# Kernel optimization log

Measured on AMD Instinct MI355X. Metric: run time of the kernel, lower is better.

Reference implementation:

```python
import jax, jax.numpy as jnp
import numpy as np

TEMPERATURE = 1.0
B, D = 8192, 256


def setup_inputs() -> dict:
    key = jax.random.key(0)
    k1, k2 = jax.random.split(key)
    return {
        "encoder_embedding1": jax.random.normal(k1, (B, D), dtype=jnp.float32),
        "encoder_embedding2": jax.random.normal(k2, (B, D), dtype=jnp.float32),
    }


def _l2_normalize(x, eps=1e-8):
    # matches torch CosineSimilarity eps handling closely enough for fp32
    n = jnp.sqrt(jnp.sum(x * x, axis=-1, keepdims=True))
    return x / jnp.maximum(n, eps)


def reference(encoder_embedding1, encoder_embedding2):
    # sim[i, j] = cos(contrast_i, anchor_j); torch builds this via a (B,B,D)
    # expand + elementwise CosineSimilarity — here it's a normalized matmul.
    a = _l2_normalize(encoder_embedding1)  # anchors  [B, D]
    c = _l2_normalize(encoder_embedding2)  # contrast [B, D]
    sim = jnp.einsum("id,jd->ij", c, a)    # [B, B]
    log_probs = jax.nn.log_softmax(sim / TEMPERATURE, axis=0)
    loss = -jnp.sum(jnp.diagonal(log_probs)) * TEMPERATURE
    return loss
```

## Files before the change

kernel.cpp:

```cpp
#include <hip/hip_runtime.h>
#include <hip/hip_bf16.h>
#include <hip/hip_fp8.h>


#define BROWS 8192
#define DIM   256

typedef int   i32x4 __attribute__((ext_vector_type(4)));
typedef int   i32x8 __attribute__((ext_vector_type(8)));
typedef float f32x4 __attribute__((ext_vector_type(4)));

__device__ __forceinline__ void gload_lds16(const void* g, void* l) {
  __builtin_amdgcn_global_load_lds(
      (const __attribute__((address_space(1))) unsigned int*)g,
      (__attribute__((address_space(3))) unsigned int*)l, 16, 0, 0);
}

__device__ __forceinline__ unsigned char to_e4m3(float v) {
  __hip_fp8_e4m3 t(v);
  return *reinterpret_cast<unsigned char*>(&t);
}

__global__ __launch_bounds__(256) void prep_kernel(
    const float* __restrict__ E1, const float* __restrict__ E2,
    unsigned char* __restrict__ An8, unsigned char* __restrict__ Cn8,
    float* __restrict__ diag, float* __restrict__ colsum) {
  if (blockIdx.x < 32) colsum[blockIdx.x * 256 + threadIdx.x] = 0.f;

  const int w    = threadIdx.x >> 6;
  const int lane = threadIdx.x & 63;
  const int row  = blockIdx.x * 4 + w;
  const size_t base = (size_t)row * DIM + lane * 4;

  const float4 a = *(const float4*)(E1 + base);
  const float4 c = *(const float4*)(E2 + base);

  float sa  = a.x*a.x + a.y*a.y + a.z*a.z + a.w*a.w;
  float sc  = c.x*c.x + c.y*c.y + c.z*c.z + c.w*c.w;
  float sac = a.x*c.x + a.y*c.y + a.z*c.z + a.w*c.w;
#pragma unroll
  for (int o = 32; o > 0; o >>= 1) {
    sa  += __shfl_down(sa,  o);
    sc  += __shfl_down(sc,  o);
    sac += __shfl_down(sac, o);
  }
  const float inva = 1.0f / fmaxf(sqrtf(__shfl(sa, 0)), 1e-8f);
  const float invc = 1.0f / fmaxf(sqrtf(__shfl(sc, 0)), 1e-8f);

  uchar4 pa, pc;
  pa.x = to_e4m3(a.x * inva); pa.y = to_e4m3(a.y * inva);
  pa.z = to_e4m3(a.z * inva); pa.w = to_e4m3(a.w * inva);
  pc.x = to_e4m3(c.x * invc); pc.y = to_e4m3(c.y * invc);
  pc.z = to_e4m3(c.z * invc); pc.w = to_e4m3(c.w * invc);
  *(uchar4*)(An8 + base) = pa;
  *(uchar4*)(Cn8 + base) = pc;
  if (lane == 0) diag[row] = sac * inva * invc;
}

__global__ __launch_bounds__(256, 2) void gemm_colsum_kernel(
    const unsigned char* __restrict__ Cn8,
    const unsigned char* __restrict__ An8,
    float* __restrict__ colsum) {
  __shared__ __align__(16) unsigned char ldsC[32768];
  __shared__ __align__(16) unsigned char ldsA[4][2][4096];

  const int tid  = threadIdx.x;
  const int lane = tid & 63;
  const int w    = tid >> 6;
  const int ih   = w & 1;
  const int js   = w >> 1;

  const int jgroup = blockIdx.x & 31;
  const int itile  = blockIdx.x >> 5;
  const int i0 = itile * 128;
  const int j0 = jgroup * 256;
  const int jw = j0 + js * 128;

  const int sr = tid >> 4;
  const int pl = (tid & 15) ^ (sr & 7);
  const unsigned char* gC = Cn8 + (size_t)(i0 + sr) * DIM + pl * 16;
#pragma unroll
  for (int r = 0; r < 8; ++r)
    gload_lds16(gC + (size_t)(r * 16) * DIM, &ldsC[0] + r * 4096 + w * 1024);

  const int srow4 = lane >> 4;
  const int slot  = lane & 15;
  const unsigned char* gA0 = An8 + (size_t)srow4 * DIM + (slot ^ srow4) * 16;
  const unsigned char* gA1 = An8 + (size_t)srow4 * DIM + (slot ^ srow4 ^ 4) * 16;
  unsigned char* wbuf = &ldsA[w][0][0];

  auto stageA = [&](int jj, int buf) {
    const size_t cb = (size_t)(jw + jj * 16) * DIM;
    unsigned char* d = wbuf + buf * 4096;
#pragma unroll
    for (int r = 0; r < 4; ++r) {
      const unsigned char* s = (r & 1) ? gA1 : gA0;
      gload_lds16(s + cb + (size_t)(r * 4) * DIM, d + r * 1024);
    }
  };

  stageA(0, 0);
  stageA(1, 1);

  asm volatile("s_waitcnt vmcnt(8)" ::: "memory");
  __builtin_amdgcn_sched_barrier(0);
  __builtin_amdgcn_s_barrier();

  const int q  = lane >> 4;
  const int rb = lane & 15;
  const int SC = 0x7F7F7F7F;

  i32x8 af[4][2];
#pragma unroll
  for (int m = 0; m < 4; ++m) {
    const int r = ih * 64 + m * 16 + rb;
#pragma unroll
    for (int W = 0; W < 2; ++W) {
      const int s0 = (W * 8 + q * 2)     ^ (r & 7);
      const int s1 = (W * 8 + q * 2 + 1) ^ (r & 7);
      union { i32x4 h[2]; i32x8 v; } u;
      u.h[0] = *(const i32x4*)(&ldsC[0] + r * 256 + s0 * 16);
      u.h[1] = *(const i32x4*)(&ldsC[0] + r * 256 + s1 * 16);
      af[m][W] = u.v;
    }
  }
  asm volatile("s_waitcnt lgkmcnt(0)" ::: "memory");
  __builtin_amdgcn_sched_barrier(0);

#pragma unroll
  for (int jj = 0; jj < 8; ++jj) {
    const int b = jj & 1;
    if (jj == 0)      asm volatile("s_waitcnt vmcnt(4)" ::: "memory");
    else if (jj == 1) asm volatile("s_waitcnt vmcnt(5)" ::: "memory");
    else if (jj == 7) asm volatile("s_waitcnt vmcnt(2)" ::: "memory");
    else              asm volatile("s_waitcnt vmcnt(6)" ::: "memory");
    __builtin_amdgcn_sched_barrier(0);

    i32x8 bf[2];
#pragma unroll
    for (int W = 0; W < 2; ++W) {
      const int s0 = (W * 8 + q * 2)     ^ (rb & 7);
      const int s1 = (W * 8 + q * 2 + 1) ^ (rb & 7);
      union { i32x4 h[2]; i32x8 v; } u;
      u.h[0] = *(const i32x4*)(wbuf + b * 4096 + rb * 256 + s0 * 16);
      u.h[1] = *(const i32x4*)(wbuf + b * 4096 + rb * 256 + s1 * 16);
      bf[W] = u.v;
    }
    asm volatile("s_waitcnt lgkmcnt(0)" ::: "memory");
    __builtin_amdgcn_sched_barrier(0);

    if (jj < 6) stageA(jj + 2, b);
    __builtin_amdgcn_sched_barrier(0);

    f32x4 acc[4] = {};
    __builtin_amdgcn_s_setprio(1);
#pragma unroll
    for (int m = 0; m < 4; ++m)
#pragma unroll
      for (int W = 0; W < 2; ++W)
        acc[m] = __builtin_amdgcn_mfma_scale_f32_16x16x128_f8f6f4(
            af[m][W], bf[W], acc[m], 0, 0, 0, SC, 0, SC);
    __builtin_amdgcn_s_setprio(0);

    float s = 0.f;
#pragma unroll
    for (int m = 0; m < 4; ++m) {
      const f32x4 v = acc[m];
      s += __expf(v[0]) + __expf(v[1]) + __expf(v[2]) + __expf(v[3]);
    }
    s += __shfl_xor(s, 16);
    s += __shfl_xor(s, 32);
    if (lane < 16) atomicAdd(&colsum[jw + jj * 16 + lane], s);
  }
}

__global__ __launch_bounds__(256) void finalize_kernel(
    const float* __restrict__ colsum, const float* __restrict__ diag,
    float* __restrict__ out) {
  const int t = threadIdx.x;
  float s = 0.f;
  for (int j = t; j < BROWS; j += 256) s += logf(colsum[j]) - diag[j];
#pragma unroll
  for (int o = 32; o > 0; o >>= 1) s += __shfl_down(s, o);
  __shared__ float red[4];
  if ((t & 63) == 0) red[t >> 6] = s;
  __syncthreads();
  if (t == 0) out[0] = red[0] + red[1] + red[2] + red[3];
}

extern "C" void kernel_launch(void* const* d_in, const int* in_sizes, int n_in,
                              void* d_out, int out_size, void* d_ws, size_t ws_size,
                              hipStream_t stream) {
  const float* E1 = (const float*)d_in[0];
  const float* E2 = (const float*)d_in[1];
  char* ws = (char*)d_ws;
  unsigned char* Cn8 = (unsigned char*)(ws);
  unsigned char* An8 = (unsigned char*)(ws + (size_t)2 * 1024 * 1024);
  float* colsum = (float*)(ws + (size_t)4 * 1024 * 1024);
  float* diag   = (float*)(ws + (size_t)4 * 1024 * 1024 + 32 * 1024);
  float* out = (float*)d_out;

  prep_kernel<<<BROWS / 4, 256, 0, stream>>>(E1, E2, An8, Cn8, diag, colsum);
  gemm_colsum_kernel<<<64 * 32, 256, 0, stream>>>(Cn8, An8, colsum);
  finalize_kernel<<<1, 256, 0, stream>>>(colsum, diag, out);
}
```

Before: 50.84 us.

## Load MFMA operands directly from global memory into registers, dropping LDS staging

The GEMM kernel no longer stages the C tile and the A sub-tiles through LDS with async global-to-LDS loads and hand-placed waitcnts. Each lane now reads its fp8 fragments straight from global memory into registers, with register double-buffering for the B operand. This removes LDS traffic, the block barrier and the swizzle arithmetic, and lets the compiler schedule the waits. In exchange it gives up cross-wave sharing of the C tile, so global/L2 reads per block go up, and the launch-bounds occupancy hint is dropped.

```diff
diff --git a/kernel.cpp b/kernel.cpp
--- a/kernel.cpp
+++ b/kernel.cpp
@@ -6,15 +6,8 @@
 #define BROWS 8192
 #define DIM   256
 
-typedef int   i32x4 __attribute__((ext_vector_type(4)));
 typedef int   i32x8 __attribute__((ext_vector_type(8)));
 typedef float f32x4 __attribute__((ext_vector_type(4)));
-
-__device__ __forceinline__ void gload_lds16(const void* g, void* l) {
-  __builtin_amdgcn_global_load_lds(
-      (const __attribute__((address_space(1))) unsigned int*)g,
-      (__attribute__((address_space(3))) unsigned int*)l, 16, 0, 0);
-}
 
 __device__ __forceinline__ unsigned char to_e4m3(float v) {
   __hip_fp8_e4m3 t(v);
@@ -57,13 +50,10 @@
   if (lane == 0) diag[row] = sac * inva * invc;
 }
 
-__global__ __launch_bounds__(256, 2) void gemm_colsum_kernel(
+__global__ __launch_bounds__(256) void gemm_colsum_kernel(
     const unsigned char* __restrict__ Cn8,
     const unsigned char* __restrict__ An8,
     float* __restrict__ colsum) {
-  __shared__ __align__(16) unsigned char ldsC[32768];
-  __shared__ __align__(16) unsigned char ldsA[4][2][4096];
-
   const int tid  = threadIdx.x;
   const int lane = tid & 63;
   const int w    = tid >> 6;
@@ -73,85 +63,30 @@
   const int jgroup = blockIdx.x & 31;
   const int itile  = blockIdx.x >> 5;
   const int i0 = itile * 128;
-  const int j0 = jgroup * 256;
-  const int jw = j0 + js * 128;
-
-  const int sr = tid >> 4;
-  const int pl = (tid & 15) ^ (sr & 7);
-  const unsigned char* gC = Cn8 + (size_t)(i0 + sr) * DIM + pl * 16;
-#pragma unroll
-  for (int r = 0; r < 8; ++r)
-    gload_lds16(gC + (size_t)(r * 16) * DIM, &ldsC[0] + r * 4096 + w * 1024);
-
-  const int srow4 = lane >> 4;
-  const int slot  = lane & 15;
-  const unsigned char* gA0 = An8 + (size_t)srow4 * DIM + (slot ^ srow4) * 16;
-  const unsigned char* gA1 = An8 + (size_t)srow4 * DIM + (slot ^ srow4 ^ 4) * 16;
-  unsigned char* wbuf = &ldsA[w][0][0];
-
-  auto stageA = [&](int jj, int buf) {
-    const size_t cb = (size_t)(jw + jj * 16) * DIM;
-    unsigned char* d = wbuf + buf * 4096;
-#pragma unroll
-    for (int r = 0; r < 4; ++r) {
-      const unsigned char* s = (r & 1) ? gA1 : gA0;
-      gload_lds16(s + cb + (size_t)(r * 4) * DIM, d + r * 1024);
-    }
-  };
-
-  stageA(0, 0);
-  stageA(1, 1);
-
-  asm volatile("s_waitcnt vmcnt(8)" ::: "memory");
-  __builtin_amdgcn_sched_barrier(0);
-  __builtin_amdgcn_s_barrier();
+  const int jw = jgroup * 256 + js * 128;
 
   const int q  = lane >> 4;
   const int rb = lane & 15;
   const int SC = 0x7F7F7F7F;
 
+  const unsigned char* cb =
+      Cn8 + (size_t)(i0 + ih * 64 + rb) * DIM + q * 32;
   i32x8 af[4][2];
 #pragma unroll
-  for (int m = 0; m < 4; ++m) {
-    const int r = ih * 64 + m * 16 + rb;
+  for (int m = 0; m < 4; ++m)
 #pragma unroll
-    for (int W = 0; W < 2; ++W) {
-      const int s0 = (W * 8 + q * 2)     ^ (r & 7);
-      const int s1 = (W * 8 + q * 2 + 1) ^ (r & 7);
-      union { i32x4 h[2]; i32x8 v; } u;
-      u.h[0] = *(const i32x4*)(&ldsC[0] + r * 256 + s0 * 16);
-      u.h[1] = *(const i32x4*)(&ldsC[0] + r * 256 + s1 * 16);
-      af[m][W] = u.v;
-    }
-  }
-  asm volatile("s_waitcnt lgkmcnt(0)" ::: "memory");
-  __builtin_amdgcn_sched_barrier(0);
+    for (int W = 0; W < 2; ++W)
+      af[m][W] = *(const i32x8*)(cb + (size_t)m * 16 * DIM + W * 128);
 
+  const unsigned char* ab = An8 + (size_t)(jw + rb) * DIM + q * 32;
+
+  auto loadB = [&](i32x8* b, int jj) {
 #pragma unroll
-  for (int jj = 0; jj < 8; ++jj) {
-    const int b = jj & 1;
-    if (jj == 0)      asm volatile("s_waitcnt vmcnt(4)" ::: "memory");
-    else if (jj == 1) asm volatile("s_waitcnt vmcnt(5)" ::: "memory");
-    else if (jj == 7) asm volatile("s_waitcnt vmcnt(2)" ::: "memory");
-    else              asm volatile("s_waitcnt vmcnt(6)" ::: "memory");
-    __builtin_amdgcn_sched_barrier(0);
+    for (int W = 0; W < 2; ++W)
+      b[W] = *(const i32x8*)(ab + (size_t)jj * 16 * DIM + W * 128);
+  };
 
-    i32x8 bf[2];
-#pragma unroll
-    for (int W = 0; W < 2; ++W) {
-      const int s0 = (W * 8 + q * 2)     ^ (rb & 7);
-      const int s1 = (W * 8 + q * 2 + 1) ^ (rb & 7);
-      union { i32x4 h[2]; i32x8 v; } u;
-      u.h[0] = *(const i32x4*)(wbuf + b * 4096 + rb * 256 + s0 * 16);
-      u.h[1] = *(const i32x4*)(wbuf + b * 4096 + rb * 256 + s1 * 16);
-      bf[W] = u.v;
-    }
-    asm volatile("s_waitcnt lgkmcnt(0)" ::: "memory");
-    __builtin_amdgcn_sched_barrier(0);
-
-    if (jj < 6) stageA(jj + 2, b);
-    __builtin_amdgcn_sched_barrier(0);
-
+  auto compute = [&](const i32x8* b, int jj) {
     f32x4 acc[4] = {};
     __builtin_amdgcn_s_setprio(1);
 #pragma unroll
@@ -159,7 +94,7 @@
 #pragma unroll
       for (int W = 0; W < 2; ++W)
         acc[m] = __builtin_amdgcn_mfma_scale_f32_16x16x128_f8f6f4(
-            af[m][W], bf[W], acc[m], 0, 0, 0, SC, 0, SC);
+            af[m][W], b[W], acc[m], 0, 0, 0, SC, 0, SC);
     __builtin_amdgcn_s_setprio(0);
 
     float s = 0.f;
@@ -171,6 +106,17 @@
     s += __shfl_xor(s, 16);
     s += __shfl_xor(s, 32);
     if (lane < 16) atomicAdd(&colsum[jw + jj * 16 + lane], s);
+  };
+
+  i32x8 b0[2], b1[2];
+  loadB(b0, 0);
+#pragma unroll
+  for (int jp = 0; jp < 4; ++jp) {
+    const int ja = jp * 2, jb = jp * 2 + 1;
+    loadB(b1, jb);
+    compute(b0, ja);
+    if (jb + 1 <= 7) loadB(b0, jb + 1);
+    compute(b1, jb);
   }
 }
 
```

Result: slower. 67.10 us (+32.0%).
